# Optimization experiments

Hardware: AMD Instinct MI355X
Metric: run time of the kernel (lower is better)

Reference implementation:

```python
import jax, jax.numpy as jnp
import numpy as np

LO = 30            # rollout horizon (hard-coded in SimCore)
AS_DIM = 400       # ssbm_actionstate_dim
HEAD = AS_DIM + 7  # per-player decoder width


def setup_inputs() -> dict:
    key = jax.random.key(0)
    ks = jax.random.split(key, 12)
    T, B, A, H = 128, 256, 64, 1024
    Nt, Ng = 6, 4
    Lu = T - 1 - LO
    s = 0.02
    return dict(
        observations=jax.random.uniform(ks[0], (T, B, 16), jnp.float32),
        actions=jax.random.normal(ks[1], (T, B, A), jnp.float32),
        beliefs=jax.random.normal(ks[2], (T, B, H), jnp.float32),
        w_ih=jax.random.normal(ks[3], (3 * H, A), jnp.float32) * s,
        w_hh=jax.random.normal(ks[4], (3 * H, H), jnp.float32) * s,
        b_ih=jnp.zeros((3 * H,), jnp.float32),
        b_hh=jnp.zeros((3 * H,), jnp.float32),
        pre_w1=jax.random.normal(ks[5], (64, H), jnp.float32) * s,
        pre_b1=jnp.zeros((64,), jnp.float32),
        pre_w2=jax.random.normal(ks[6], (H, 64), jnp.float32) * s,
        pre_b2=jnp.zeros((H,), jnp.float32),
        dec_w=jax.random.normal(ks[7], (2 * HEAD, H), jnp.float32) * s,
        dec_b=jnp.zeros((2 * HEAD,), jnp.float32),
        idx_i=jax.random.randint(ks[8], (Nt,), 0, Lu, dtype=jnp.int32),
        K=jax.random.randint(ks[9], (Nt, Ng), 0, LO, dtype=jnp.int32),
    )


def _bce_logits(x, t):
    # binary_cross_entropy_with_logits, elementwise
    return jax.nn.softplus(x) - x * t


def _player_loss(pred, tgt):
    # pred: [Nt,Ng,B,407] logits; tgt: [Nt,Ng,B,8] observation half
    # pytorch means are over everything except the Nt python loop -> mean over (Ng,B[,feat])
    logits = pred[..., :AS_DIM]
    cls = tgt[..., 0].astype(jnp.int32)                     # .long() of float target
    ce = -jnp.take_along_axis(jax.nn.log_softmax(logits, -1), cls[..., None], -1)[..., 0]
    loss = ce.mean(axis=(1, 2))
    loss = loss + ((pred[..., 400:402] - tgt[..., 1:3]) ** 2).mean(axis=(1, 2, 3))
    loss = loss + ((jax.nn.softplus(pred[..., 402:403]) - tgt[..., 3:4]) ** 2).mean(axis=(1, 2, 3))
    loss = loss + ((jax.nn.softplus(pred[..., 403:404]) - tgt[..., 4:5]) ** 2).mean(axis=(1, 2, 3))
    loss = loss + _bce_logits(pred[..., 404:405], tgt[..., 5:6]).mean(axis=(1, 2, 3))
    loss = loss + _bce_logits(pred[..., 405:406], tgt[..., 6:7]).mean(axis=(1, 2, 3))
    loss = loss + _bce_logits(pred[..., 406:407], tgt[..., 7:8]).mean(axis=(1, 2, 3))
    return loss  # [Nt]


def reference(observations, actions, beliefs, w_ih, w_hh, b_ih, b_hh,
              pre_w1, pre_b1, pre_w2, pre_b2, dec_w, dec_b, idx_i, K):
    def gru_cell(h, a):
        gi = a @ w_ih.T + b_ih              # [B,3H]
        gh = h @ w_hh.T + b_hh
        ir, iz, in_ = jnp.split(gi, 3, axis=-1)
        hr, hz, hn = jnp.split(gh, 3, axis=-1)
        r = jax.nn.sigmoid(ir + hr)
        z = jax.nn.sigmoid(iz + hz)
        n = jnp.tanh(in_ + r * hn)
        h_new = (1.0 - z) * n + z * h
        return h_new, h_new

    def rollout(i, k):
        h0 = beliefs[i]                                          # [B,H]
        acts = jax.lax.dynamic_slice_in_dim(actions, i, LO, axis=0)
        _, states = jax.lax.scan(gru_cell, h0, acts)             # [Lo,B,H]
        return states[k], observations[k + i + 1]                # [Ng,B,H],[Ng,B,16]

    states, obs = jax.vmap(rollout)(idx_i, K)                    # [Nt,Ng,B,H]

    # ResidualBlock: x + relu(relu(x W1^T + b1) W2^T + b2)
    h = jax.nn.relu(states @ pre_w1.T + pre_b1)
    x = states + jax.nn.relu(h @ pre_w2.T + pre_b2)

    logits = x @ dec_w.T + dec_b                                 # [Nt,Ng,B,814]
    agent, opponent = logits[..., :HEAD], logits[..., HEAD:]
    tgt_a, tgt_o = obs[..., :8], obs[..., 8:]

    loss = (_player_loss(agent, tgt_a) + _player_loss(opponent, tgt_o)).sum()
    return loss
```

## Files before the change

kernel.cpp:

```cpp
#include <hip/hip_runtime.h>
#include <hip/hip_bf16.h>

typedef __bf16 bf16;
typedef __attribute__((ext_vector_type(4))) __bf16 bf16x4;
typedef __attribute__((ext_vector_type(8))) __bf16 bf16x8;
typedef __attribute__((ext_vector_type(4))) float f32x4;

static __device__ __forceinline__ f32x4 MFMA(bf16x8 a, bf16x8 b, f32x4 c) {
  return __builtin_amdgcn_mfma_f32_16x16x32_bf16(a, b, c, 0, 0, 0);
}

__device__ __forceinline__ float sigm(float x) { return 1.0f / (1.0f + __expf(-x)); }
__device__ __forceinline__ float softplus_(float x) {
  return fmaxf(x, 0.0f) + log1pf(__expf(-fabsf(x)));
}

__device__ __forceinline__ void gl16(const bf16* g, char* l) {
  __builtin_amdgcn_global_load_lds(
      (const __attribute__((address_space(1))) char*)g,
      (__attribute__((address_space(3))) char*)l, 16, 0, 0);
}

__global__ void k_prep(const float* __restrict__ whh, const float* __restrict__ wih,
                       const float* __restrict__ act, const float* __restrict__ w1,
                       const float* __restrict__ w2, const float* __restrict__ dw,
                       const float* __restrict__ beliefs, const int* __restrict__ idx_i,
                       bf16* __restrict__ Whd, bf16* __restrict__ Wid,
                       bf16* __restrict__ actd, bf16* __restrict__ w1d,
                       bf16* __restrict__ w2d, bf16* __restrict__ dwd,
                       bf16* __restrict__ hAd) {
  for (int q = blockIdx.x * blockDim.x + threadIdx.x; q < 1994240;
       q += gridDim.x * blockDim.x) {
    const float* src;
    bf16* dst;
    int off;
    if (q < 786432)       { src = whh; dst = Whd;  off = q; }
    else if (q < 835584)  { src = wih; dst = Wid;  off = q - 786432; }
    else if (q < 1359872) { src = act; dst = actd; off = q - 835584; }
    else if (q < 1376256) { src = w1;  dst = w1d;  off = q - 1359872; }
    else if (q < 1392640) { src = w2;  dst = w2d;  off = q - 1376256; }
    else if (q < 1601024) { src = dw;  dst = dwd;  off = q - 1392640; }
    else {
      const int e = (q - 1601024) << 2;
      const int n = e >> 18, rest = e & 262143;
      float4 v = *(const float4*)&beliefs[((size_t)idx_i[n] << 18) + rest];
      bf16x4 o = {(bf16)v.x, (bf16)v.y, (bf16)v.z, (bf16)v.w};
      *(bf16x4*)&hAd[e] = o;
      continue;
    }
    float4 v = *(const float4*)&src[(size_t)off << 2];
    bf16x4 o = {(bf16)v.x, (bf16)v.y, (bf16)v.z, (bf16)v.w};
    *(bf16x4*)&dst[(size_t)off << 2] = o;
  }
}

__global__ __launch_bounds__(256, 2) void k_gru_step(
    const bf16* __restrict__ hin, bf16* __restrict__ hout,
    const bf16* __restrict__ Wh, const bf16* __restrict__ Wi,
    const bf16* __restrict__ actB,
    const float* __restrict__ b_ih, const float* __restrict__ b_hh,
    const int* __restrict__ idx_i, const int* __restrict__ Kmat,
    bf16* __restrict__ states, int step) {
  const int pid = blockIdx.x;
  const int xcd = pid & 7;
  const int rg = xcd >> 2;
  const int cgp = xcd & 3;
  const int q = pid >> 3;
  const int mtl = q & 7;
  const int jtl = q >> 3;
  const int m0 = rg * 768 + mtl * 96;
  const int j0 = (cgp * 8 + jtl) * 32;

  const int tid = threadIdx.x, wave = tid >> 6, lane = tid & 63;
  const int l15 = lane & 15;
  const int kgrp = lane >> 4;
  const int wm = wave >> 1;
  const int wj = wave & 1;
  const int jlane = j0 + wj * 16 + l15;

  __shared__ alignas(16) bf16 As[3][96][64];
  __shared__ alignas(16) bf16 Bs[3][96][64];

  const int srow = lane >> 3;
  const int scol = (((lane & 7) ^ srow) << 3);

  const bf16* asrc[3];
  const bf16* bsrc[3];
  const bf16* aisrc[3];
  const bf16* bisrc[3];
#pragma unroll
  for (int i = 0; i < 3; ++i) {
    const int prow = wave * 24 + i * 8 + srow;
    const int grow = m0 + prow;
    asrc[i] = hin + (size_t)grow * 1024 + scol;
    const int wr = (prow >> 5) * 1024 + j0 + (prow & 31);
    bsrc[i] = Wh + (size_t)wr * 1024 + scol;
    bisrc[i] = Wi + (size_t)wr * 64 + scol;
    const int np = grow >> 8;
    aisrc[i] = actB + ((size_t)(idx_i[np] + step) * 256 + (grow & 255)) * 64 + scol;
  }

  auto stage = [&](int buf, int it) {
    char* ad = (char*)As + buf * 12288 + (wave * 24) * 128;
    char* bd = (char*)Bs + buf * 12288 + (wave * 24) * 128;
    if (it < 16) {
#pragma unroll
      for (int i = 0; i < 3; ++i) {
        gl16(asrc[i] + it * 64, ad + i * 1024);
        gl16(bsrc[i] + it * 64, bd + i * 1024);
      }
    } else {
#pragma unroll
      for (int i = 0; i < 3; ++i) {
        gl16(aisrc[i], ad + i * 1024);
        gl16(bisrc[i], bd + i * 1024);
      }
    }
  };

  f32x4 accR[3], accZ[3], accNh[3], accNi[3];
  const f32x4 zero = {0.f, 0.f, 0.f, 0.f};
#pragma unroll
  for (int f = 0; f < 3; ++f) { accR[f] = zero; accZ[f] = zero; accNh[f] = zero; accNi[f] = zero; }

  const float br = b_ih[jlane] + b_hh[jlane];
  const float bz = b_ih[1024 + jlane] + b_hh[1024 + jlane];
  const float bin = b_ih[2048 + jlane];
  const float bhn = b_hh[2048 + jlane];

  auto compute = [&](int buf, f32x4 (&gN)[3]) {
    const char* ab = (const char*)As + buf * 12288;
    const char* bb = (const char*)Bs + buf * 12288;
#pragma unroll
    for (int kkI = 0; kkI < 2; ++kkI) {
      const int kbyte = (((kkI << 5) + (kgrp << 3)) << 1) ^ ((l15 & 7) << 4);
      bf16x8 a0 = *(const bf16x8*)(ab + (wm * 48 + l15) * 128 + kbyte);
      bf16x8 a1 = *(const bf16x8*)(ab + (wm * 48 + 16 + l15) * 128 + kbyte);
      bf16x8 a2 = *(const bf16x8*)(ab + (wm * 48 + 32 + l15) * 128 + kbyte);
      bf16x8 b_r = *(const bf16x8*)(bb + (wj * 16 + l15) * 128 + kbyte);
      bf16x8 b_z = *(const bf16x8*)(bb + (32 + wj * 16 + l15) * 128 + kbyte);
      bf16x8 b_n = *(const bf16x8*)(bb + (64 + wj * 16 + l15) * 128 + kbyte);
      accR[0] = MFMA(a0, b_r, accR[0]);
      accR[1] = MFMA(a1, b_r, accR[1]);
      accR[2] = MFMA(a2, b_r, accR[2]);
      accZ[0] = MFMA(a0, b_z, accZ[0]);
      accZ[1] = MFMA(a1, b_z, accZ[1]);
      accZ[2] = MFMA(a2, b_z, accZ[2]);
      gN[0] = MFMA(a0, b_n, gN[0]);
      gN[1] = MFMA(a1, b_n, gN[1]);
      gN[2] = MFMA(a2, b_n, gN[2]);
    }
  };

  stage(0, 0);
  stage(1, 1);

  uint2 hpreg[3];

#pragma unroll
  for (int t = 0; t < 17; ++t) {
    if (t < 15) stage((t + 2) % 3, t + 2);
    if (t == 14) {
#pragma unroll
      for (int it2 = 0; it2 < 3; ++it2) {
        const int u = it2 * 256 + tid;
        const int row = u >> 3, c = u & 7;
        hpreg[it2] = *(const uint2*)(hin + (size_t)(m0 + row) * 1024 + j0 + c * 4);
      }
    }
    if (t <= 13)      asm volatile("s_waitcnt vmcnt(12)" ::: "memory");
    else if (t == 14) asm volatile("s_waitcnt vmcnt(15)" ::: "memory");
    else if (t == 15) asm volatile("s_waitcnt vmcnt(9)" ::: "memory");
    else              asm volatile("s_waitcnt vmcnt(0)" ::: "memory");
    __builtin_amdgcn_s_barrier();
    if (t == 16) compute(1, accNi);
    else         compute(t % 3, accNh);
    __builtin_amdgcn_sched_barrier(0);
    __builtin_amdgcn_s_barrier();
  }

  bf16* Hp = (bf16*)&As[0][0][0];
  bf16* Hn = (bf16*)&Bs[0][0][0];

#pragma unroll
  for (int it2 = 0; it2 < 3; ++it2) {
    const int u = it2 * 256 + tid;
    const int row = u >> 3, c = u & 7;
    *(uint2*)&Hp[row * 40 + c * 4] = hpreg[it2];
  }
  __syncthreads();

#pragma unroll
  for (int mf = 0; mf < 3; ++mf) {
#pragma unroll
    for (int ii = 0; ii < 4; ++ii) {
      const int ml = wm * 48 + mf * 16 + kgrp * 4 + ii;
      const int jl = wj * 16 + l15;
      float hp = (float)Hp[ml * 40 + jl];
      float rg2 = sigm(accR[mf][ii] + br);
      float zg = sigm(accZ[mf][ii] + bz);
      float ng = tanhf(accNi[mf][ii] + bin + rg2 * (accNh[mf][ii] + bhn));
      float hnew = (1.0f - zg) * ng + zg * hp;
      Hn[ml * 40 + jl] = (bf16)hnew;
    }
  }
  __syncthreads();

#pragma unroll
  for (int it2 = 0; it2 < 3; ++it2) {
    const int u = it2 * 256 + tid;
    const int row = u >> 3, c = u & 7;
    const int m = m0 + row;
    uint2 v = *(const uint2*)&Hn[row * 40 + c * 4];
    *(uint2*)&hout[(size_t)m * 1024 + j0 + c * 4] = v;
    const int n = m >> 8;
    const int b = m & 255;
#pragma unroll
    for (int g = 0; g < 4; ++g) {
      if (Kmat[n * 4 + g] == step)
        *(uint2*)&states[((size_t)(n * 4 + g) * 256 + b) * 1024 + j0 + c * 4] = v;
    }
  }
}

template <int EPI, int SWZ>
__global__ __launch_bounds__(256) void k_gemm_epi(
    const bf16* __restrict__ A, const bf16* __restrict__ W, int K, int Nreal, int ld_out,
    const float* __restrict__ bias, const bf16* __restrict__ resid,
    float* __restrict__ outF, bf16* __restrict__ outB) {
  int mt, jt;
  if (SWZ) {
    const int lin = blockIdx.x;
    const int x = lin & 7, k = lin >> 3;
    mt = 12 * x + k % 12;
    jt = k / 12;
  } else {
    mt = blockIdx.x;
    jt = blockIdx.y;
  }
  const int m0 = mt * 64;
  const int j0 = jt * 64;
  const int tid = threadIdx.x, wave = tid >> 6, lane = tid & 63;
  __shared__ alignas(16) bf16 Al[64][72];
  __shared__ alignas(16) bf16 Wl[64][72];

  f32x4 acc[4];
  const f32x4 zero = {0.f, 0.f, 0.f, 0.f};
#pragma unroll
  for (int f = 0; f < 4; ++f) acc[f] = zero;

  const int r = tid >> 3, c8 = (tid & 7) << 3;
  const int arow = wave * 16 + (lane & 15);
  const int koff = (lane >> 4) << 3;

  for (int kb = 0; kb < K; kb += 64) {
    *(bf16x8*)&Al[r][c8]      = *(const bf16x8*)&A[(size_t)(m0 + r) * K + kb + c8];
    *(bf16x8*)&Al[r + 32][c8] = *(const bf16x8*)&A[(size_t)(m0 + r + 32) * K + kb + c8];
    int jr = j0 + r;      if (jr >= Nreal) jr = Nreal - 1;
    int jr2 = j0 + r + 32; if (jr2 >= Nreal) jr2 = Nreal - 1;
    *(bf16x8*)&Wl[r][c8]      = *(const bf16x8*)&W[(size_t)jr * K + kb + c8];
    *(bf16x8*)&Wl[r + 32][c8] = *(const bf16x8*)&W[(size_t)jr2 * K + kb + c8];
    __syncthreads();
#pragma unroll
    for (int kk = 0; kk < 64; kk += 32) {
      bf16x8 av = *(const bf16x8*)&Al[arow][kk + koff];
#pragma unroll
      for (int nf = 0; nf < 4; ++nf) {
        acc[nf] = MFMA(av, *(const bf16x8*)&Wl[nf * 16 + (lane & 15)][kk + koff], acc[nf]);
      }
    }
    __syncthreads();
  }

#pragma unroll
  for (int nf = 0; nf < 4; ++nf) {
    int j = j0 + nf * 16 + (lane & 15);
    float bj = (j < Nreal) ? bias[j] : 0.f;
#pragma unroll
    for (int i = 0; i < 4; ++i) {
      int m = m0 + wave * 16 + ((lane >> 4) << 2) + i;
      float v = acc[nf][i] + bj;
      if (EPI == 0) {
        outB[(size_t)m * ld_out + j] = (bf16)fmaxf(v, 0.f);
      } else if (EPI == 1) {
        v = fmaxf(v, 0.f) + (float)resid[(size_t)m * ld_out + j];
        outB[(size_t)m * ld_out + j] = (bf16)v;
      } else {
        if (j < Nreal) outF[(size_t)m * ld_out + j] = v;
      }
    }
  }
}

__global__ __launch_bounds__(256) void k_loss_rows(
    const float* __restrict__ logits, const float* __restrict__ obs,
    const int* __restrict__ idx_i, const int* __restrict__ Kmat,
    float* __restrict__ partials) {
  const int row = blockIdx.x;
  const int n = row >> 10, g = (row >> 8) & 3, b = row & 255;
  const int i = idx_i[n], k = Kmat[n * 4 + g];
  const float* L = logits + (size_t)row * 814;
  const float* ob = obs + ((size_t)(k + i + 1) * 256 + b) * 16;
  const int tid = threadIdx.x, lane = tid & 63, wv = tid >> 6;
  __shared__ float red[4];

  float total = 0.f;
#pragma unroll
  for (int p = 0; p < 2; ++p) {
    const float* Lp = L + p * 407;
    const float* tg = ob + p * 8;
    float mx = -1e30f;
    for (int c = tid; c < 400; c += 256) mx = fmaxf(mx, Lp[c]);
#pragma unroll
    for (int s = 32; s; s >>= 1) mx = fmaxf(mx, __shfl_xor(mx, s));
    __syncthreads();
    if (lane == 0) red[wv] = mx;
    __syncthreads();
    mx = fmaxf(fmaxf(red[0], red[1]), fmaxf(red[2], red[3]));
    __syncthreads();
    float se = 0.f;
    for (int c = tid; c < 400; c += 256) se += __expf(Lp[c] - mx);
#pragma unroll
    for (int s = 32; s; s >>= 1) se += __shfl_xor(se, s);
    if (lane == 0) red[wv] = se;
    __syncthreads();
    se = red[0] + red[1] + red[2] + red[3];
    __syncthreads();

    if (tid == 0) {
      int cls = (int)tg[0];
      float lse = mx + logf(se);
      float v = lse - Lp[cls];
      float d0 = Lp[400] - tg[1], d1 = Lp[401] - tg[2];
      v += 0.5f * (d0 * d0 + d1 * d1);
      float s2 = softplus_(Lp[402]) - tg[3]; v += s2 * s2;
      float s3 = softplus_(Lp[403]) - tg[4]; v += s3 * s3;
      v += softplus_(Lp[404]) - Lp[404] * tg[5];
      v += softplus_(Lp[405]) - Lp[405] * tg[6];
      v += softplus_(Lp[406]) - Lp[406] * tg[7];
      total += v;
    }
    __syncthreads();
  }
  if (tid == 0) partials[row] = total * (1.0f / 1024.0f);
}

__global__ void k_reduce_final(const float* __restrict__ partials, float* __restrict__ out) {
  __shared__ float s[256];
  float v = 0.f;
  for (int i = threadIdx.x; i < 6144; i += 256) v += partials[i];
  s[threadIdx.x] = v;
  __syncthreads();
  for (int st = 128; st; st >>= 1) {
    if (threadIdx.x < st) s[threadIdx.x] += s[threadIdx.x + st];
    __syncthreads();
  }
  if (threadIdx.x == 0) out[0] = s[0];
}


extern "C" void kernel_launch(void* const* d_in, const int* in_sizes, int n_in,
                              void* d_out, int out_size, void* d_ws, size_t ws_size,
                              hipStream_t stream) {
  const float* obs      = (const float*)d_in[0];
  const float* actions  = (const float*)d_in[1];
  const float* beliefs  = (const float*)d_in[2];
  const float* w_ih     = (const float*)d_in[3];
  const float* w_hh     = (const float*)d_in[4];
  const float* b_ih     = (const float*)d_in[5];
  const float* b_hh     = (const float*)d_in[6];
  const float* pre_w1   = (const float*)d_in[7];
  const float* pre_b1   = (const float*)d_in[8];
  const float* pre_w2   = (const float*)d_in[9];
  const float* pre_b2   = (const float*)d_in[10];
  const float* dec_w    = (const float*)d_in[11];
  const float* dec_b    = (const float*)d_in[12];
  const int*   idx_i    = (const int*)d_in[13];
  const int*   Kmat     = (const int*)d_in[14];
  float* outF = (float*)d_out;

  char* p = (char*)d_ws;
  auto carve = [&](size_t bytes) {
    char* q = p;
    p += (bytes + 255) & ~(size_t)255;
    return q;
  };
  bf16* Wh      = (bf16*)carve(3072u * 1024u * 2u);
  bf16* Wi      = (bf16*)carve(3072u * 64u * 2u);
  bf16* actBv   = (bf16*)carve(128u * 256u * 64u * 2u);
  bf16* preW1b  = (bf16*)carve(64u * 1024u * 2u);
  bf16* preW2b  = (bf16*)carve(1024u * 64u * 2u);
  bf16* decWb   = (bf16*)carve(814u * 1024u * 2u);
  bf16* hA      = (bf16*)carve(1536u * 1024u * 2u);
  bf16* hB      = (bf16*)carve(1536u * 1024u * 2u);
  bf16* states  = (bf16*)carve(6144u * 1024u * 2u);
  bf16* h1      = (bf16*)carve(6144u * 64u * 2u);
  bf16* xbuf    = (bf16*)carve(6144u * 1024u * 2u);
  float* logits = (float*)carve((size_t)6144u * 814u * 4u);
  float* partials = (float*)carve(6144u * 4u);

  k_prep<<<2048, 256, 0, stream>>>(w_hh, w_ih, actions, pre_w1, pre_w2, dec_w,
                                   beliefs, idx_i, Wh, Wi, actBv, preW1b, preW2b,
                                   decWb, hA);

  for (int t = 0; t < 30; ++t) {
    const bf16* hi = (t & 1) ? hB : hA;
    bf16* ho = (t & 1) ? hA : hB;
    k_gru_step<<<512, 256, 0, stream>>>(hi, ho, Wh, Wi, actBv, b_ih, b_hh,
                                        idx_i, Kmat, states, t);
  }

  k_gemm_epi<0, 0><<<dim3(96, 1), 256, 0, stream>>>(states, preW1b, 1024, 64, 64,
                                                    pre_b1, nullptr, nullptr, h1);
  k_gemm_epi<1, 1><<<1536, 256, 0, stream>>>(h1, preW2b, 64, 1024, 1024,
                                             pre_b2, states, nullptr, xbuf);
  k_gemm_epi<2, 1><<<1248, 256, 0, stream>>>(xbuf, decWb, 1024, 814, 814,
                                             dec_b, nullptr, logits, nullptr);

  k_loss_rows<<<6144, 256, 0, stream>>>(logits, obs, idx_i, Kmat, partials);
  k_reduce_final<<<1, 256, 0, stream>>>(partials, outF);
}
```

Before: 660.2 us.

## Widen GRU step tiles to 64 columns with split load waves, fuse final reduction

Each GRU step block now covers a 96x64 output tile with 512 threads instead of 96x32 with 256. Four waves stage the hidden-state A tiles and four stage the weight B tiles, and wave priority is raised around the MFMA sections. This doubles reuse of the staged A tile and halves the grid, but lowers occupancy and roughly doubles LDS per block. The separate final reduction kernel is removed: the last loss block, found by an atomic counter that k_prep resets, sums the partials, which saves one launch.

```diff
diff --git a/kernel.cpp b/kernel.cpp
--- a/kernel.cpp
+++ b/kernel.cpp
@@ -28,7 +28,8 @@
                        bf16* __restrict__ Whd, bf16* __restrict__ Wid,
                        bf16* __restrict__ actd, bf16* __restrict__ w1d,
                        bf16* __restrict__ w2d, bf16* __restrict__ dwd,
-                       bf16* __restrict__ hAd) {
+                       bf16* __restrict__ hAd, unsigned* __restrict__ cnt) {
+  if (blockIdx.x == 0 && threadIdx.x == 0) *cnt = 0u;
   for (int q = blockIdx.x * blockDim.x + threadIdx.x; q < 1994240;
        q += gridDim.x * blockDim.x) {
     const float* src;
@@ -54,7 +55,7 @@
   }
 }
 
-__global__ __launch_bounds__(256, 2) void k_gru_step(
+__global__ __launch_bounds__(512, 1) void k_gru_step(
     const bf16* __restrict__ hin, bf16* __restrict__ hout,
     const bf16* __restrict__ Wh, const bf16* __restrict__ Wi,
     const bf16* __restrict__ actB,
@@ -69,51 +70,61 @@
   const int mtl = q & 7;
   const int jtl = q >> 3;
   const int m0 = rg * 768 + mtl * 96;
-  const int j0 = (cgp * 8 + jtl) * 32;
+  const int j0 = (cgp * 4 + jtl) * 64;
 
   const int tid = threadIdx.x, wave = tid >> 6, lane = tid & 63;
   const int l15 = lane & 15;
   const int kgrp = lane >> 4;
-  const int wm = wave >> 1;
-  const int wj = wave & 1;
-  const int jlane = j0 + wj * 16 + l15;
+  const int wm = wave >> 2;
+  const int wjj = wave & 3;
+  const int jlane = j0 + wjj * 16 + l15;
 
   __shared__ alignas(16) bf16 As[3][96][64];
-  __shared__ alignas(16) bf16 Bs[3][96][64];
+  __shared__ alignas(16) bf16 Bs[3][192][64];
 
   const int srow = lane >> 3;
   const int scol = (((lane & 7) ^ srow) << 3);
 
-  const bf16* asrc[3];
-  const bf16* bsrc[3];
-  const bf16* aisrc[3];
-  const bf16* bisrc[3];
-#pragma unroll
-  for (int i = 0; i < 3; ++i) {
-    const int prow = wave * 24 + i * 8 + srow;
-    const int grow = m0 + prow;
-    asrc[i] = hin + (size_t)grow * 1024 + scol;
-    const int wr = (prow >> 5) * 1024 + j0 + (prow & 31);
-    bsrc[i] = Wh + (size_t)wr * 1024 + scol;
-    bisrc[i] = Wi + (size_t)wr * 64 + scol;
-    const int np = grow >> 8;
-    aisrc[i] = actB + ((size_t)(idx_i[np] + step) * 256 + (grow & 255)) * 64 + scol;
+  const bf16* asrc[3];  const bf16* aisrc[3];
+  const bf16* bsrc[6];  const bf16* bisrc[6];
+  if (wave < 4) {
+#pragma unroll
+    for (int i = 0; i < 3; ++i) {
+      const int prow = wave * 24 + i * 8 + srow;
+      const int grow = m0 + prow;
+      asrc[i] = hin + (size_t)grow * 1024 + scol;
+      const int np = grow >> 8;
+      aisrc[i] = actB + ((size_t)(idx_i[np] + step) * 256 + (grow & 255)) * 64 + scol;
+    }
+  } else {
+    const int w4 = wave - 4;
+#pragma unroll
+    for (int i = 0; i < 6; ++i) {
+      const int p = w4 * 48 + i * 8 + srow;
+      const int wr = (p >> 6) * 1024 + j0 + (p & 63);
+      bsrc[i] = Wh + (size_t)wr * 1024 + scol;
+      bisrc[i] = Wi + (size_t)wr * 64 + scol;
+    }
   }
 
   auto stage = [&](int buf, int it) {
-    char* ad = (char*)As + buf * 12288 + (wave * 24) * 128;
-    char* bd = (char*)Bs + buf * 12288 + (wave * 24) * 128;
-    if (it < 16) {
-#pragma unroll
-      for (int i = 0; i < 3; ++i) {
-        gl16(asrc[i] + it * 64, ad + i * 1024);
-        gl16(bsrc[i] + it * 64, bd + i * 1024);
+    if (wave < 4) {
+      char* ad = (char*)As + buf * 12288 + (wave * 24) * 128;
+      if (it < 16) {
+#pragma unroll
+        for (int i = 0; i < 3; ++i) gl16(asrc[i] + it * 64, ad + i * 1024);
+      } else {
+#pragma unroll
+        for (int i = 0; i < 3; ++i) gl16(aisrc[i], ad + i * 1024);
       }
     } else {
-#pragma unroll
-      for (int i = 0; i < 3; ++i) {
-        gl16(aisrc[i], ad + i * 1024);
-        gl16(bisrc[i], bd + i * 1024);
+      char* bd = (char*)Bs + buf * 24576 + ((wave - 4) * 48) * 128;
+      if (it < 16) {
+#pragma unroll
+        for (int i = 0; i < 6; ++i) gl16(bsrc[i] + it * 64, bd + i * 1024);
+      } else {
+#pragma unroll
+        for (int i = 0; i < 6; ++i) gl16(bisrc[i], bd + i * 1024);
       }
     }
   };
@@ -130,16 +141,17 @@
 
   auto compute = [&](int buf, f32x4 (&gN)[3]) {
     const char* ab = (const char*)As + buf * 12288;
-    const char* bb = (const char*)Bs + buf * 12288;
+    const char* bb = (const char*)Bs + buf * 24576;
+    __builtin_amdgcn_s_setprio(1);
 #pragma unroll
     for (int kkI = 0; kkI < 2; ++kkI) {
       const int kbyte = (((kkI << 5) + (kgrp << 3)) << 1) ^ ((l15 & 7) << 4);
       bf16x8 a0 = *(const bf16x8*)(ab + (wm * 48 + l15) * 128 + kbyte);
       bf16x8 a1 = *(const bf16x8*)(ab + (wm * 48 + 16 + l15) * 128 + kbyte);
       bf16x8 a2 = *(const bf16x8*)(ab + (wm * 48 + 32 + l15) * 128 + kbyte);
-      bf16x8 b_r = *(const bf16x8*)(bb + (wj * 16 + l15) * 128 + kbyte);
-      bf16x8 b_z = *(const bf16x8*)(bb + (32 + wj * 16 + l15) * 128 + kbyte);
-      bf16x8 b_n = *(const bf16x8*)(bb + (64 + wj * 16 + l15) * 128 + kbyte);
+      bf16x8 b_r = *(const bf16x8*)(bb + (wjj * 16 + l15) * 128 + kbyte);
+      bf16x8 b_z = *(const bf16x8*)(bb + (64 + wjj * 16 + l15) * 128 + kbyte);
+      bf16x8 b_n = *(const bf16x8*)(bb + (128 + wjj * 16 + l15) * 128 + kbyte);
       accR[0] = MFMA(a0, b_r, accR[0]);
       accR[1] = MFMA(a1, b_r, accR[1]);
       accR[2] = MFMA(a2, b_r, accR[2]);
@@ -150,6 +162,7 @@
       gN[1] = MFMA(a1, b_n, gN[1]);
       gN[2] = MFMA(a2, b_n, gN[2]);
     }
+    __builtin_amdgcn_s_setprio(0);
   };
 
   stage(0, 0);
@@ -163,15 +176,23 @@
     if (t == 14) {
 #pragma unroll
       for (int it2 = 0; it2 < 3; ++it2) {
-        const int u = it2 * 256 + tid;
-        const int row = u >> 3, c = u & 7;
+        const int u = it2 * 512 + tid;
+        const int row = u >> 4, c = u & 15;
         hpreg[it2] = *(const uint2*)(hin + (size_t)(m0 + row) * 1024 + j0 + c * 4);
       }
     }
-    if (t <= 13)      asm volatile("s_waitcnt vmcnt(12)" ::: "memory");
-    else if (t == 14) asm volatile("s_waitcnt vmcnt(15)" ::: "memory");
-    else if (t == 15) asm volatile("s_waitcnt vmcnt(9)" ::: "memory");
-    else              asm volatile("s_waitcnt vmcnt(0)" ::: "memory");
+    if (t <= 13) {
+      if (wave < 4) asm volatile("s_waitcnt vmcnt(6)" ::: "memory");
+      else          asm volatile("s_waitcnt vmcnt(12)" ::: "memory");
+    } else if (t == 14) {
+      if (wave < 4) asm volatile("s_waitcnt vmcnt(9)" ::: "memory");
+      else          asm volatile("s_waitcnt vmcnt(15)" ::: "memory");
+    } else if (t == 15) {
+      if (wave < 4) asm volatile("s_waitcnt vmcnt(6)" ::: "memory");
+      else          asm volatile("s_waitcnt vmcnt(9)" ::: "memory");
+    } else {
+      asm volatile("s_waitcnt vmcnt(3)" ::: "memory");
+    }
     __builtin_amdgcn_s_barrier();
     if (t == 16) compute(1, accNi);
     else         compute(t % 3, accNh);
@@ -179,14 +200,14 @@
     __builtin_amdgcn_s_barrier();
   }
 
-  bf16* Hp = (bf16*)&As[0][0][0];
-  bf16* Hn = (bf16*)&Bs[0][0][0];
+  bf16* Hp = (bf16*)&Bs[0][0][0];
+  bf16* Hn = (bf16*)&Bs[1][0][0];
 
 #pragma unroll
   for (int it2 = 0; it2 < 3; ++it2) {
-    const int u = it2 * 256 + tid;
-    const int row = u >> 3, c = u & 7;
-    *(uint2*)&Hp[row * 40 + c * 4] = hpreg[it2];
+    const int u = it2 * 512 + tid;
+    const int row = u >> 4, c = u & 15;
+    *(uint2*)&Hp[row * 72 + c * 4] = hpreg[it2];
   }
   __syncthreads();
 
@@ -195,23 +216,23 @@
 #pragma unroll
     for (int ii = 0; ii < 4; ++ii) {
       const int ml = wm * 48 + mf * 16 + kgrp * 4 + ii;
-      const int jl = wj * 16 + l15;
-      float hp = (float)Hp[ml * 40 + jl];
+      const int jl = wjj * 16 + l15;
+      float hp = (float)Hp[ml * 72 + jl];
       float rg2 = sigm(accR[mf][ii] + br);
       float zg = sigm(accZ[mf][ii] + bz);
       float ng = tanhf(accNi[mf][ii] + bin + rg2 * (accNh[mf][ii] + bhn));
       float hnew = (1.0f - zg) * ng + zg * hp;
-      Hn[ml * 40 + jl] = (bf16)hnew;
+      Hn[ml * 72 + jl] = (bf16)hnew;
     }
   }
   __syncthreads();
 
 #pragma unroll
   for (int it2 = 0; it2 < 3; ++it2) {
-    const int u = it2 * 256 + tid;
-    const int row = u >> 3, c = u & 7;
+    const int u = it2 * 512 + tid;
+    const int row = u >> 4, c = u & 15;
     const int m = m0 + row;
-    uint2 v = *(const uint2*)&Hn[row * 40 + c * 4];
+    uint2 v = *(const uint2*)&Hn[row * 72 + c * 4];
     *(uint2*)&hout[(size_t)m * 1024 + j0 + c * 4] = v;
     const int n = m >> 8;
     const int b = m & 255;
@@ -295,7 +316,7 @@
 __global__ __launch_bounds__(256) void k_loss_rows(
     const float* __restrict__ logits, const float* __restrict__ obs,
     const int* __restrict__ idx_i, const int* __restrict__ Kmat,
-    float* __restrict__ partials) {
+    float* __restrict__ partials, float* __restrict__ out, unsigned* __restrict__ cnt) {
   const int row = blockIdx.x;
   const int n = row >> 10, g = (row >> 8) & 3, b = row & 255;
   const int i = idx_i[n], k = Kmat[n * 4 + g];
@@ -342,20 +363,23 @@
     }
     __syncthreads();
   }
-  if (tid == 0) partials[row] = total * (1.0f / 1024.0f);
-}
-
-__global__ void k_reduce_final(const float* __restrict__ partials, float* __restrict__ out) {
-  __shared__ float s[256];
-  float v = 0.f;
-  for (int i = threadIdx.x; i < 6144; i += 256) v += partials[i];
-  s[threadIdx.x] = v;
+  __shared__ unsigned lastv;
+  if (tid == 0) {
+    partials[row] = total * (1.0f / 1024.0f);
+    __threadfence();
+    lastv = atomicAdd(cnt, 1u);
+  }
   __syncthreads();
-  for (int st = 128; st; st >>= 1) {
-    if (threadIdx.x < st) s[threadIdx.x] += s[threadIdx.x + st];
-    __syncthreads();
-  }
-  if (threadIdx.x == 0) out[0] = s[0];
+  if (lastv == 6143u) {
+    __threadfence();
+    float v = 0.f;
+    for (int idx = tid; idx < 6144; idx += 256) v += partials[idx];
+#pragma unroll
+    for (int s = 32; s; s >>= 1) v += __shfl_xor(v, s);
+    if (lane == 0) red[wv] = v;
+    __syncthreads();
+    if (tid == 0) out[0] = red[0] + red[1] + red[2] + red[3];
+  }
 }
 
 
@@ -398,15 +422,16 @@
   bf16* xbuf    = (bf16*)carve(6144u * 1024u * 2u);
   float* logits = (float*)carve((size_t)6144u * 814u * 4u);
   float* partials = (float*)carve(6144u * 4u);
+  unsigned* cnt  = (unsigned*)carve(256u);
 
   k_prep<<<2048, 256, 0, stream>>>(w_hh, w_ih, actions, pre_w1, pre_w2, dec_w,
                                    beliefs, idx_i, Wh, Wi, actBv, preW1b, preW2b,
-                                   decWb, hA);
+                                   decWb, hA, cnt);
 
   for (int t = 0; t < 30; ++t) {
     const bf16* hi = (t & 1) ? hB : hA;
     bf16* ho = (t & 1) ? hA : hB;
-    k_gru_step<<<512, 256, 0, stream>>>(hi, ho, Wh, Wi, actBv, b_ih, b_hh,
+    k_gru_step<<<256, 512, 0, stream>>>(hi, ho, Wh, Wi, actBv, b_ih, b_hh,
                                         idx_i, Kmat, states, t);
   }
 
@@ -417,6 +442,5 @@
   k_gemm_epi<2, 1><<<1248, 256, 0, stream>>>(xbuf, decWb, 1024, 814, 814,
                                              dec_b, nullptr, logits, nullptr);
 
-  k_loss_rows<<<6144, 256, 0, stream>>>(logits, obs, idx_i, Kmat, partials);
-  k_reduce_final<<<1, 256, 0, stream>>>(partials, outF);
-}
+  k_loss_rows<<<6144, 256, 0, stream>>>(logits, obs, idx_i, Kmat, partials, outF, cnt);
+}
```

Measured after the change: 726.7 us. +10.1%, slower.

## Skip GRU steps beyond needed horizon and use wave-per-row loss kernel

Applied to the files above, without the earlier changes.

Each GRU step block reads the K indices for the rollouts its row tile covers and exits early when the current step exceeds the largest needed K, avoiding recurrent matmuls whose states are never consumed. The loss kernel is rewritten so that one wavefront handles one player half of a row, with all values held in registers and only shuffle reductions, which removes the shared-memory barriers. The partial-sum buffer doubles in size to hold per-half results. The early exit depends on K at runtime, so the savings vary with the input.

```diff
diff --git a/kernel.cpp b/kernel.cpp
--- a/kernel.cpp
+++ b/kernel.cpp
@@ -71,6 +71,21 @@
   const int m0 = rg * 768 + mtl * 96;
   const int j0 = (cgp * 8 + jtl) * 32;
 
+  {
+    const int nlo = m0 >> 8, nhi = (m0 + 95) >> 8;
+    int mk = Kmat[nlo * 4 + 0];
+    mk = max(mk, Kmat[nlo * 4 + 1]);
+    mk = max(mk, Kmat[nlo * 4 + 2]);
+    mk = max(mk, Kmat[nlo * 4 + 3]);
+    if (nhi != nlo) {
+      mk = max(mk, Kmat[nhi * 4 + 0]);
+      mk = max(mk, Kmat[nhi * 4 + 1]);
+      mk = max(mk, Kmat[nhi * 4 + 2]);
+      mk = max(mk, Kmat[nhi * 4 + 3]);
+    }
+    if (step > mk) return;
+  }
+
   const int tid = threadIdx.x, wave = tid >> 6, lane = tid & 63;
   const int l15 = lane & 15;
   const int kgrp = lane >> 4;
@@ -292,63 +307,55 @@
   }
 }
 
-__global__ __launch_bounds__(256) void k_loss_rows(
+__global__ __launch_bounds__(256) void k_loss_wave(
     const float* __restrict__ logits, const float* __restrict__ obs,
     const int* __restrict__ idx_i, const int* __restrict__ Kmat,
     float* __restrict__ partials) {
-  const int row = blockIdx.x;
+  const int gw = blockIdx.x * 4 + (threadIdx.x >> 6);
+  const int lane = threadIdx.x & 63;
+  const int row = gw >> 1, p = gw & 1;
   const int n = row >> 10, g = (row >> 8) & 3, b = row & 255;
   const int i = idx_i[n], k = Kmat[n * 4 + g];
-  const float* L = logits + (size_t)row * 814;
-  const float* ob = obs + ((size_t)(k + i + 1) * 256 + b) * 16;
-  const int tid = threadIdx.x, lane = tid & 63, wv = tid >> 6;
-  __shared__ float red[4];
-
-  float total = 0.f;
-#pragma unroll
-  for (int p = 0; p < 2; ++p) {
-    const float* Lp = L + p * 407;
-    const float* tg = ob + p * 8;
-    float mx = -1e30f;
-    for (int c = tid; c < 400; c += 256) mx = fmaxf(mx, Lp[c]);
-#pragma unroll
-    for (int s = 32; s; s >>= 1) mx = fmaxf(mx, __shfl_xor(mx, s));
-    __syncthreads();
-    if (lane == 0) red[wv] = mx;
-    __syncthreads();
-    mx = fmaxf(fmaxf(red[0], red[1]), fmaxf(red[2], red[3]));
-    __syncthreads();
-    float se = 0.f;
-    for (int c = tid; c < 400; c += 256) se += __expf(Lp[c] - mx);
-#pragma unroll
-    for (int s = 32; s; s >>= 1) se += __shfl_xor(se, s);
-    if (lane == 0) red[wv] = se;
-    __syncthreads();
-    se = red[0] + red[1] + red[2] + red[3];
-    __syncthreads();
-
-    if (tid == 0) {
-      int cls = (int)tg[0];
-      float lse = mx + logf(se);
-      float v = lse - Lp[cls];
-      float d0 = Lp[400] - tg[1], d1 = Lp[401] - tg[2];
-      v += 0.5f * (d0 * d0 + d1 * d1);
-      float s2 = softplus_(Lp[402]) - tg[3]; v += s2 * s2;
-      float s3 = softplus_(Lp[403]) - tg[4]; v += s3 * s3;
-      v += softplus_(Lp[404]) - Lp[404] * tg[5];
-      v += softplus_(Lp[405]) - Lp[405] * tg[6];
-      v += softplus_(Lp[406]) - Lp[406] * tg[7];
-      total += v;
-    }
-    __syncthreads();
-  }
-  if (tid == 0) partials[row] = total * (1.0f / 1024.0f);
+  const float* Lp = logits + (size_t)row * 814 + p * 407;
+  const float* tg = obs + ((size_t)(k + i + 1) * 256 + b) * 16 + p * 8;
+
+  float v[7];
+#pragma unroll
+  for (int it = 0; it < 7; ++it) {
+    const int c = lane + it * 64;
+    v[it] = (c < 400) ? Lp[c] : -1e30f;
+  }
+  float mx = fmaxf(fmaxf(fmaxf(v[0], v[1]), fmaxf(v[2], v[3])),
+                   fmaxf(fmaxf(v[4], v[5]), v[6]));
+#pragma unroll
+  for (int s = 32; s; s >>= 1) mx = fmaxf(mx, __shfl_xor(mx, s));
+  float se = 0.f;
+#pragma unroll
+  for (int it = 0; it < 7; ++it) {
+    const int c = lane + it * 64;
+    se += (c < 400) ? __expf(v[it] - mx) : 0.f;
+  }
+#pragma unroll
+  for (int s = 32; s; s >>= 1) se += __shfl_xor(se, s);
+
+  if (lane == 0) {
+    const int cls = (int)tg[0];
+    float val = mx + logf(se) - Lp[cls];
+    const float d0 = Lp[400] - tg[1], d1 = Lp[401] - tg[2];
+    val += 0.5f * (d0 * d0 + d1 * d1);
+    const float s2 = softplus_(Lp[402]) - tg[3]; val += s2 * s2;
+    const float s3 = softplus_(Lp[403]) - tg[4]; val += s3 * s3;
+    val += softplus_(Lp[404]) - Lp[404] * tg[5];
+    val += softplus_(Lp[405]) - Lp[405] * tg[6];
+    val += softplus_(Lp[406]) - Lp[406] * tg[7];
+    partials[gw] = val * (1.0f / 1024.0f);
+  }
 }
 
 __global__ void k_reduce_final(const float* __restrict__ partials, float* __restrict__ out) {
   __shared__ float s[256];
   float v = 0.f;
-  for (int i = threadIdx.x; i < 6144; i += 256) v += partials[i];
+  for (int i = threadIdx.x; i < 12288; i += 256) v += partials[i];
   s[threadIdx.x] = v;
   __syncthreads();
   for (int st = 128; st; st >>= 1) {
@@ -397,7 +404,7 @@
   bf16* h1      = (bf16*)carve(6144u * 64u * 2u);
   bf16* xbuf    = (bf16*)carve(6144u * 1024u * 2u);
   float* logits = (float*)carve((size_t)6144u * 814u * 4u);
-  float* partials = (float*)carve(6144u * 4u);
+  float* partials = (float*)carve(12288u * 4u);
 
   k_prep<<<2048, 256, 0, stream>>>(w_hh, w_ih, actions, pre_w1, pre_w2, dec_w,
                                    beliefs, idx_i, Wh, Wi, actBv, preW1b, preW2b,
@@ -417,6 +424,6 @@
   k_gemm_epi<2, 1><<<1248, 256, 0, stream>>>(xbuf, decWb, 1024, 814, 814,
                                              dec_b, nullptr, logits, nullptr);
 
-  k_loss_rows<<<6144, 256, 0, stream>>>(logits, obs, idx_i, Kmat, partials);
+  k_loss_wave<<<3072, 256, 0, stream>>>(logits, obs, idx_i, Kmat, partials);
   k_reduce_final<<<1, 256, 0, stream>>>(partials, outF);
 }
```

After: 665.8 us. About the same (+0.9%).
